# Kernel optimization log

Measured on AMD Instinct MI355X. Metric: run time of the kernel, lower is better.

## Reference

```python
import jax, jax.numpy as jnp
import numpy as np
from jax import lax

B, T, IN, H, DIM = 128, 1024, 64, 128, 64


def setup_inputs() -> dict:
    key = jax.random.key(0)
    ks = jax.random.split(key, 14)
    s = 0.05
    return {
        "x": jax.random.normal(ks[0], (B, T, IN), jnp.float32),
        "is_init": jax.random.randint(ks[1], (B, T, 1), 0, 2).astype(bool),
        "hx": jax.random.normal(ks[2], (B, H), jnp.float32),
        # MLP: Linear(IN,128) + ELU, Linear(128,128) + ELU
        "W1": jax.random.normal(ks[3], (128, IN), jnp.float32) * s,
        "b1": jnp.zeros((128,), jnp.float32),
        "W2": jax.random.normal(ks[4], (128, 128), jnp.float32) * s,
        "b2": jnp.zeros((128,), jnp.float32),
        # GRU params (torch layout: [3H, in] with gate order r,z,n)
        "W_ih": jax.random.normal(ks[5], (3 * H, 128), jnp.float32) * s,
        "b_ih": jnp.zeros((3 * H,), jnp.float32),
        "W_hh": jax.random.normal(ks[6], (3 * H, H), jnp.float32) * s,
        "b_hh": jnp.zeros((3 * H,), jnp.float32),
        # output head Linear(128, DIM)
        "W_out": jax.random.normal(ks[7], (DIM, 128), jnp.float32) * s,
        "b_out": jnp.zeros((DIM,), jnp.float32),
    }


def _gru_with_reset(xg, init_mask, h0, W_hh, b_hh):
    # xg: [T,B,3H] precomputed input-side gates; init_mask: [T,B,1] float
    def step(h, inp):
        xg_t, m_t = inp
        h = h * (1.0 - m_t)                       # reset hidden where is_init
        hg = h @ W_hh.T + b_hh                    # [B,3H]
        xr, xz, xn = jnp.split(xg_t, 3, axis=-1)
        hr, hz, hn = jnp.split(hg, 3, axis=-1)
        r = jax.nn.sigmoid(xr + hr)
        z = jax.nn.sigmoid(xz + hz)
        n = jnp.tanh(xn + r * hn)
        h_new = (1.0 - z) * n + z * h
        return h_new, h_new

    hT, ys = lax.scan(step, h0, (xg, init_mask))
    return ys, hT


def reference(x, is_init, hx, W1, b1, W2, b2, W_ih, b_ih, W_hh, b_hh, W_out, b_out):
    # MLP (ELU activations)
    h = jax.nn.elu(x @ W1.T + b1)
    h = jax.nn.elu(h @ W2.T + b2)                 # [B,T,128]
    # precompute input-side gate projections for all timesteps (one big GEMM)
    xg = h @ W_ih.T + b_ih                        # [B,T,3H]
    xg_t = jnp.transpose(xg, (1, 0, 2))           # [T,B,3H]
    m_t = jnp.transpose(is_init.astype(x.dtype), (1, 0, 2))  # [T,B,1]
    ys, hT = _gru_with_reset(xg_t, m_t, hx, W_hh, b_hh)
    y = jnp.transpose(ys, (1, 0, 2))              # [B,T,H]
    out = y @ W_out.T + b_out                     # [B,T,DIM]
    return out, hT
```

## Files before the change

### kernel.cpp

```cpp
#include <hip/hip_runtime.h>


#define T_SZ 1024

typedef __attribute__((ext_vector_type(8))) short short8;
typedef __attribute__((ext_vector_type(4))) float f32x4;
typedef unsigned long long u64;
typedef unsigned int uint32;

__device__ __forceinline__ unsigned short f2b(float f){
  return __builtin_bit_cast(unsigned short, (__bf16)f);
}
__device__ __forceinline__ float b2f(unsigned int hs){
  unsigned int u = hs << 16;
  return __builtin_bit_cast(float, u);
}
__device__ __forceinline__ short8 load_w8(const float* __restrict__ p){
  const float4* q = (const float4*)p;
  float4 u0 = q[0], u1 = q[1];
  short8 v;
  v[0]=(short)f2b(u0.x); v[1]=(short)f2b(u0.y); v[2]=(short)f2b(u0.z); v[3]=(short)f2b(u0.w);
  v[4]=(short)f2b(u1.x); v[5]=(short)f2b(u1.y); v[6]=(short)f2b(u1.z); v[7]=(short)f2b(u1.w);
  return v;
}
__device__ __forceinline__ float rcp_f(float x){ return __builtin_amdgcn_rcpf(x); }
__device__ __forceinline__ float elu(float v){ return v > 0.f ? v : __expf(v) - 1.f; }
__device__ __forceinline__ float sigm(float x){ return rcp_f(1.f + __expf(-x)); }
__device__ __forceinline__ float tanh_fast(float x){
  x = fminf(fmaxf(x, -15.f), 15.f);
  float e = __expf(-2.f * x);
  return (1.f - e) * rcp_f(1.f + e);
}
#define MFMA16(a,b,c) __builtin_amdgcn_mfma_f32_16x16x32_bf16(a, b, c, 0, 0, 0)


__global__ __launch_bounds__(512) void wprep(const float* __restrict__ Whh, uint4* __restrict__ wbf){
  int rec = blockIdx.x*512 + threadIdx.x;
  if(rec >= 6144) return;
  int q  = rec & 3;
  int n_ = (rec >> 2) & 127;
  int ks = (rec >> 9) & 3;
  int gt = rec >> 11;
  const float* p = Whh + (size_t)(n_ + 128*gt)*128 + ks*32 + q*8;
  uint4 o;
  o.x = (uint32)f2b(p[0]) | ((uint32)f2b(p[1]) << 16);
  o.y = (uint32)f2b(p[2]) | ((uint32)f2b(p[3]) << 16);
  o.z = (uint32)f2b(p[4]) | ((uint32)f2b(p[5]) << 16);
  o.w = (uint32)f2b(p[6]) | ((uint32)f2b(p[7]) << 16);
  wbf[rec] = o;
}

__global__ __launch_bounds__(512) void seg_build(const int* __restrict__ ii, uint32* C){
  __shared__ uint32 lh[1024];
  __shared__ uint32 lbase[1024];
  __shared__ uint32 ssum[512];
  __shared__ uint32 sbase;
  uint32* segs = C + 4096;
  const int tid = threadIdx.x;
  const int wv = tid >> 6, lane = tid & 63;
  const int b = blockIdx.x*8 + wv;

  for(int i = tid; i < 1024; i += 512) lh[i] = 0u;
  __syncthreads();

  u64 bal[16], mb[16];
  #pragma unroll
  for(int c=0;c<16;c++){
    int t = c*64 + lane;
    int m = ii[b*T_SZ + t];
    mb[c]  = __ballot(m != 0);
    bal[c] = __ballot((m != 0) || (t == 0));
  }
  int fsA[16]; int nx = T_SZ;
  #pragma unroll
  for(int c=15;c>=0;c--){ fsA[c]=nx; if(bal[c]) nx = c*64 + __builtin_ctzll(bal[c]); }

  int lenA[16], tA[16], rkA[16];
  #pragma unroll
  for(int c=0;c<16;c++){
    lenA[c] = 0;
    if((bal[c] >> lane) & 1ull){
      int t = c*64 + lane;
      u64 hi = (lane < 63) ? (bal[c] >> (lane+1)) : 0ull;
      int nxt = hi ? (t + 1 + __builtin_ctzll(hi)) : fsA[c];
      int len = nxt - t;
      int rst = (int)((mb[c] >> lane) & 1ull);
      len -= rst; t += rst;
      if(len > 0){
        lenA[c] = len; tA[c] = t;
        rkA[c] = (int)atomicAdd(&lh[1024 - len], 1u);
      }
    }
  }
  __syncthreads();

  uint32 c0 = lh[2*tid], c1 = lh[2*tid+1];
  ssum[tid] = c0 + c1;
  __syncthreads();
  #pragma unroll
  for(int off=1; off<512; off<<=1){
    uint32 v = (tid >= off) ? ssum[tid-off] : 0u;
    __syncthreads();
    ssum[tid] += v;
    __syncthreads();
  }
  uint32 excl = tid ? ssum[tid-1] : 0u;
  lbase[2*tid]   = excl;
  lbase[2*tid+1] = excl + c0;
  uint32 total = ssum[511];
  uint32 padded = (total + 15u) & ~15u;
  if(tid == 0){
    sbase = atomicAdd(&C[2], padded);
    atomicAdd(&C[1], padded >> 4);
  }
  __syncthreads();
  const uint32 base = sbase;

  #pragma unroll
  for(int c=0;c<16;c++){
    if(lenA[c] > 0){
      uint32 slot = base + lbase[1024 - lenA[c]] + (uint32)rkA[c];
      segs[slot] = ((uint32)b << 21) | ((uint32)tA[c] << 11) | (uint32)lenA[c];
    }
  }
  for(uint32 i = total + tid; i < padded; i += 512) segs[base + i] = 0u;
}

__global__ __launch_bounds__(512) void fused_mlp(
    const float* __restrict__ x, const int* __restrict__ ii,
    const float* __restrict__ W1, const float* __restrict__ b1,
    const float* __restrict__ W2, const float* __restrict__ b2,
    const float* __restrict__ Wih, const float* __restrict__ bih,
    const float* __restrict__ bhh,
    unsigned short* __restrict__ xg, unsigned short* __restrict__ ys,
    float* __restrict__ hT)
{
  __shared__ __align__(16) char smem[71680];
  unsigned short* xs0 = (unsigned short*)smem;
  unsigned short* xs1 = (unsigned short*)(smem + 18432);
  unsigned short* h1l = (unsigned short*)(smem + 36864);
  unsigned short* h2l = (unsigned short*)(smem + 54272);
  __shared__ int iil[2][64];
  const int tid = threadIdx.x;
  const int wv = tid >> 6, l = tid & 63, quad = l >> 4, col = l & 15;
  const int n = 16*wv + col;

  short8 w1f[2], w2f[4], wif[3][4];
  #pragma unroll
  for(int ks=0; ks<2; ks++) w1f[ks] = load_w8(W1 + n*64  + ks*32 + quad*8);
  #pragma unroll
  for(int ks=0; ks<4; ks++) w2f[ks] = load_w8(W2 + n*128 + ks*32 + quad*8);
  #pragma unroll
  for(int gt=0; gt<3; gt++){
    #pragma unroll
    for(int ks=0; ks<4; ks++)
      wif[gt][ks] = load_w8(Wih + (n + 128*gt)*128 + ks*32 + quad*8);
  }
  const float b1v = b1[n], b2v = b2[n];
  float bihv[3], bhhv[3];
  #pragma unroll
  for(int gt=0; gt<3; gt++){ bihv[gt] = bih[n + 128*gt]; bhhv[gt] = bhh[n + 128*gt]; }

  const int srow = tid >> 5, sk = tid & 31;

  auto stage3 = [&](int g3, int t03, const int* __restrict__ iilp){
    uint32 xgo[4];
    #pragma unroll
    for(int r=0; r<4; r++)
      xgo[r] = (((uint32)(16*g3 + quad*4 + r) << 10) + (uint32)t03) * 384u + (uint32)n;
    #pragma unroll
    for(int tt=0; tt<4; tt++){
      f32x4 a0 = {bihv[0], bihv[0], bihv[0], bihv[0]};
      f32x4 a1 = {bihv[1], bihv[1], bihv[1], bihv[1]};
      f32x4 a2 = {bihv[2], bihv[2], bihv[2], bihv[2]};
      #pragma unroll
      for(int ks=0; ks<4; ks++){
        short8 a = *(const short8*)&h2l[(tt*16 + col)*136 + ks*32 + quad*8];
        a0 = MFMA16(a, wif[0][ks], a0);
        a1 = MFMA16(a, wif[1][ks], a1);
        a2 = MFMA16(a, wif[2][ks], a2);
      }
      const int t = t03 + tt;
      #pragma unroll
      for(int r=0; r<4; r++){
        int row = quad*4 + r;
        unsigned short* p = xg + xgo[r] + (uint32)(tt*384);
        p[0]   = f2b(a0[r]);
        p[128] = f2b(a1[r]);
        p[256] = f2b(a2[r]);
        if(iilp[tt*16 + row] != 0){
          float rr = sigm(a0[r] + bhhv[0]);
          float zz = sigm(a1[r] + bhhv[1]);
          float nn = tanh_fast(a2[r] + rr*bhhv[2]);
          float h1 = (1.f - zz)*nn;
          ys[((size_t)(t*8 + g3)*16 + row)*128 + n] = f2b(h1);
          if(t == T_SZ-1)
            hT[(16*g3 + row)*128 + n] = h1;
        }
      }
    }
  };

  int have_prev = 0, pg = 0, pt0 = 0, p = 0;
  for(int tile = blockIdx.x; tile < 2048; tile += gridDim.x){
    const int g = tile & 7, t0 = (tile >> 3) * 4;
    unsigned short* xs = p ? xs1 : xs0;
    const float* src = x + (size_t)(16*g + srow)*(T_SZ*64) + (size_t)t0*64;
    float4 v0 = ((const float4*)src)[sk];
    float4 v1 = ((const float4*)src)[sk + 32];
    int iv = 0;
    if(tid < 64) iv = ii[(16*g + (tid & 15))*T_SZ + t0 + (tid >> 4)];
    if(have_prev) stage3(pg, pt0, iil[p^1]);
    {
      int s0 = sk, tt0 = s0 >> 4, k0 = (s0 & 15)*4;
      unsigned short* d0 = xs + (tt0*16 + srow)*72 + k0;
      d0[0]=f2b(v0.x); d0[1]=f2b(v0.y); d0[2]=f2b(v0.z); d0[3]=f2b(v0.w);
      int s1 = sk + 32, tt1 = s1 >> 4, k1 = (s1 & 15)*4;
      unsigned short* d1 = xs + (tt1*16 + srow)*72 + k1;
      d1[0]=f2b(v1.x); d1[1]=f2b(v1.y); d1[2]=f2b(v1.z); d1[3]=f2b(v1.w);
    }
    if(tid < 64) iil[p][tid] = iv;
    __syncthreads();
    #pragma unroll
    for(int tt=0; tt<4; tt++){
      f32x4 acc = {b1v, b1v, b1v, b1v};
      #pragma unroll
      for(int ks=0; ks<2; ks++){
        short8 a = *(const short8*)&xs[(tt*16 + col)*72 + ks*32 + quad*8];
        acc = MFMA16(a, w1f[ks], acc);
      }
      #pragma unroll
      for(int r=0; r<4; r++)
        h1l[(tt*16 + quad*4 + r)*136 + n] = f2b(elu(acc[r]));
    }
    __syncthreads();
    #pragma unroll
    for(int tt=0; tt<4; tt++){
      f32x4 acc = {b2v, b2v, b2v, b2v};
      #pragma unroll
      for(int ks=0; ks<4; ks++){
        short8 a = *(const short8*)&h1l[(tt*16 + col)*136 + ks*32 + quad*8];
        acc = MFMA16(a, w2f[ks], acc);
      }
      #pragma unroll
      for(int r=0; r<4; r++)
        h2l[(tt*16 + quad*4 + r)*136 + n] = f2b(elu(acc[r]));
    }
    __syncthreads();
    have_prev = 1; pg = g; pt0 = t0; p ^= 1;
  }
  if(have_prev) stage3(pg, pt0, iil[p^1]);
}

__global__ __launch_bounds__(512) void gru_seg_scan(
    const unsigned short* __restrict__ xg,
    const float* __restrict__ hx,
    const uint4* __restrict__ wbf, const float* __restrict__ bhh,
    const uint32* __restrict__ C,
    unsigned short* __restrict__ ys, float* __restrict__ hT)
{
  __shared__ unsigned short hl[2][16*136];
  __shared__ unsigned short xbuf[2][16*772];
  __shared__ int srb[16], srt[16], srlen[16];
  const uint32 ntile = C[1];
  const uint32 tile = blockIdx.x;
  if(tile >= ntile) return;

  const int tid = threadIdx.x;
  const int wv = tid >> 6, l = tid & 63, quad = l >> 4, col = l & 15;
  const int nidx = 16*wv + col;
  const int frow = tid >> 5, fk = tid & 31;
  const uint32* segs = C + 4096;

  short8 whf[3][4];
  float bhv[3];
  #pragma unroll
  for(int gt=0; gt<3; gt++){
    bhv[gt] = bhh[nidx + 128*gt];
    #pragma unroll
    for(int ks=0; ks<4; ks++){
      uint4 w = wbf[((gt*4 + ks)*128 + nidx)*4 + quad];
      whf[gt][ks] = __builtin_bit_cast(short8, w);
    }
  }

  if(tid < 16){
    uint32 w = segs[16*tile + (uint32)tid];
    srb[tid] = (int)(w >> 21);
    srt[tid] = (int)((w >> 11) & 1023u);
    srlen[tid] = (int)(w & 2047u);
  }
  __syncthreads();
  const int maxlen = srlen[0];
  const int fb = srb[frow], ft = srt[frow], fl = srlen[frow];

  float hreg[4];
  #pragma unroll
  for(int r=0; r<4; r++){
    int row = quad*4 + r;
    int b = srb[row], t0 = srt[row];
    float h0 = 0.f;
    if(srlen[row] > 0){
      h0 = (t0 == 0) ? hx[b*128 + nidx]
                     : b2f(ys[((size_t)((t0-1)*8 + (b>>4))*16 + (b&15))*128 + nidx]);
    }
    hreg[r] = h0;
    hl[0][row*136 + nidx] = f2b(h0);
  }
  {
    const unsigned short* src = xg + ((size_t)fb*T_SZ + ft)*384;
    unsigned short* xb = &xbuf[0][frow*772];
    #pragma unroll
    for(int i2=0; i2<3; i2++)
      *(u64*)(xb + i2*128 + fk*4) = *(const u64*)(src + i2*128 + fk*4);
  }

  int cur = 0;
  for(int i=0; i<maxlen; i++){
    __syncthreads();
    short8 af[4];
    #pragma unroll
    for(int ks=0; ks<4; ks++)
      af[ks] = *(const short8*)&hl[cur][col*136 + ks*32 + quad*8];
    f32x4 ar = {bhv[0], bhv[0], bhv[0], bhv[0]};
    f32x4 az = {bhv[1], bhv[1], bhv[1], bhv[1]};
    f32x4 an = {bhv[2], bhv[2], bhv[2], bhv[2]};
    #pragma unroll
    for(int ks=0; ks<4; ks++){
      ar = MFMA16(af[ks], whf[0][ks], ar);
      az = MFMA16(af[ks], whf[1][ks], az);
      an = MFMA16(af[ks], whf[2][ks], an);
    }
    u64 p0, p1, p2;
    {
      int tc = (i+1 < fl) ? i+1 : (fl > 0 ? fl-1 : 0);
      const unsigned short* src = xg + ((size_t)fb*T_SZ + (ft + tc))*384;
      p0 = *(const u64*)(src +       fk*4);
      p1 = *(const u64*)(src + 128 + fk*4);
      p2 = *(const u64*)(src + 256 + fk*4);
    }
    if(i >= 1 && i <= fl){
      int t = ft + i - 1;
      u64 hv = *(const u64*)&hl[cur][frow*136 + fk*4];
      *(u64*)(ys + ((size_t)(t*8 + (fb>>4))*16 + (fb&15))*128 + fk*4) = hv;
      if(i == fl && ft + fl == T_SZ){
        #pragma unroll
        for(int j=0; j<4; j++)
          hT[fb*128 + fk*4 + j] = b2f(hl[cur][frow*136 + fk*4 + j]);
      }
    }
    const unsigned short* xb = &xbuf[cur][0];
    #pragma unroll
    for(int r=0; r<4; r++){
      int row = quad*4 + r;
      float xrv = b2f(xb[row*772 +       nidx]);
      float xzv = b2f(xb[row*772 + 128 + nidx]);
      float xnv = b2f(xb[row*772 + 256 + nidx]);
      float rr = sigm(xrv + ar[r]);
      float zz = sigm(xzv + az[r]);
      float nn = tanh_fast(xnv + rr*an[r]);
      float hnew = (1.f - zz)*nn + zz*hreg[r];
      hreg[r] = hnew;
      hl[cur^1][row*136 + nidx] = f2b(hnew);
    }
    {
      unsigned short* xb2 = &xbuf[cur^1][frow*772];
      *(u64*)(xb2 +       fk*4) = p0;
      *(u64*)(xb2 + 128 + fk*4) = p1;
      *(u64*)(xb2 + 256 + fk*4) = p2;
    }
    cur ^= 1;
  }
  __syncthreads();
  if(maxlen >= 1 && fl == maxlen){
    int t = ft + maxlen - 1;
    u64 hv = *(const u64*)&hl[cur][frow*136 + fk*4];
    *(u64*)(ys + ((size_t)(t*8 + (fb>>4))*16 + (fb&15))*128 + fk*4) = hv;
    if(ft + fl == T_SZ){
      #pragma unroll
      for(int j=0; j<4; j++)
        hT[fb*128 + fk*4 + j] = b2f(hl[cur][frow*136 + fk*4 + j]);
    }
  }
}

__global__ __launch_bounds__(256) void out_gemm(
    const unsigned short* __restrict__ ys,
    const float* __restrict__ Wout, const float* __restrict__ bout,
    float* __restrict__ outp)
{
  const int tid = threadIdx.x;
  const int wv = tid >> 6, l = tid & 63, quad = l >> 4, col = l & 15;
  const int n = 16*wv + col;
  short8 wof[4];
  #pragma unroll
  for(int ks=0; ks<4; ks++) wof[ks] = load_w8(Wout + n*128 + ks*32 + quad*8);
  const float bov = bout[n];
  for(int tile = blockIdx.x; tile < 8192; tile += gridDim.x){
    const int t = tile >> 3, g = tile & 7;
    const unsigned short* yt = ys + (size_t)tile * 16 * 128;
    f32x4 acc = {bov, bov, bov, bov};
    #pragma unroll
    for(int ks=0; ks<4; ks++){
      short8 a = *(const short8*)&yt[col*128 + ks*32 + quad*8];
      acc = MFMA16(a, wof[ks], acc);
    }
    #pragma unroll
    for(int r=0; r<4; r++)
      outp[(size_t)(16*g + quad*4 + r)*(T_SZ*64) + (size_t)t*64 + n] = acc[r];
  }
}

extern "C" void kernel_launch(void* const* d_in, const int* in_sizes, int n_in,
                              void* d_out, int out_size, void* d_ws, size_t ws_size,
                              hipStream_t stream)
{
  const float* x    = (const float*)d_in[0];
  const int*   ii   = (const int*)  d_in[1];
  const float* hx   = (const float*)d_in[2];
  const float* W1   = (const float*)d_in[3];
  const float* b1   = (const float*)d_in[4];
  const float* W2   = (const float*)d_in[5];
  const float* b2   = (const float*)d_in[6];
  const float* Wih  = (const float*)d_in[7];
  const float* bih  = (const float*)d_in[8];
  const float* Whh  = (const float*)d_in[9];
  const float* bhh  = (const float*)d_in[10];
  const float* Wout = (const float*)d_in[11];
  const float* bout = (const float*)d_in[12];

  float* outp = (float*)d_out;
  float* hT   = outp + (size_t)128 * T_SZ * 64;
  uint32* C   = (uint32*)d_out;
  uint4* wbf  = (uint4*)((char*)d_out + (1u<<20));

  unsigned short* xg = (unsigned short*)d_ws;
  unsigned short* ys = (unsigned short*)((char*)d_ws + 100663296ull);

  hipMemsetAsync(C, 0, 64, stream);
  wprep      <<<dim3(12),   dim3(512),  0, stream>>>(Whh, wbf);
  seg_build  <<<dim3(16),   dim3(512),  0, stream>>>(ii, C);
  fused_mlp  <<<dim3(512),  dim3(512),  0, stream>>>(x, ii, W1, b1, W2, b2, Wih, bih, bhh, xg, ys, hT);
  gru_seg_scan<<<dim3(4160),dim3(512),  0, stream>>>(xg, hx, wbf, bhh, C, ys, hT);
  out_gemm   <<<dim3(2048), dim3(256),  0, stream>>>(ys, Wout, bout, outp);
}
```

Before: 235.0 us.

## Merge prep kernels, prebake bf16 weights, skip xg stores, shrink LDS, tune scan barrier

New measurement: 221.0 us. 1.06x faster.

```diff
diff --git a/kernel.cpp b/kernel.cpp
--- a/kernel.cpp
+++ b/kernel.cpp
@@ -14,14 +14,6 @@
 __device__ __forceinline__ float b2f(unsigned int hs){
   unsigned int u = hs << 16;
   return __builtin_bit_cast(float, u);
-}
-__device__ __forceinline__ short8 load_w8(const float* __restrict__ p){
-  const float4* q = (const float4*)p;
-  float4 u0 = q[0], u1 = q[1];
-  short8 v;
-  v[0]=(short)f2b(u0.x); v[1]=(short)f2b(u0.y); v[2]=(short)f2b(u0.z); v[3]=(short)f2b(u0.w);
-  v[4]=(short)f2b(u1.x); v[5]=(short)f2b(u1.y); v[6]=(short)f2b(u1.z); v[7]=(short)f2b(u1.w);
-  return v;
 }
 __device__ __forceinline__ float rcp_f(float x){ return __builtin_amdgcn_rcpf(x); }
 __device__ __forceinline__ float elu(float v){ return v > 0.f ? v : __expf(v) - 1.f; }
@@ -34,104 +26,128 @@
 #define MFMA16(a,b,c) __builtin_amdgcn_mfma_f32_16x16x32_bf16(a, b, c, 0, 0, 0)
 
 
-__global__ __launch_bounds__(512) void wprep(const float* __restrict__ Whh, uint4* __restrict__ wbf){
-  int rec = blockIdx.x*512 + threadIdx.x;
-  if(rec >= 6144) return;
-  int q  = rec & 3;
-  int n_ = (rec >> 2) & 127;
-  int ks = (rec >> 9) & 3;
-  int gt = rec >> 11;
-  const float* p = Whh + (size_t)(n_ + 128*gt)*128 + ks*32 + q*8;
-  uint4 o;
-  o.x = (uint32)f2b(p[0]) | ((uint32)f2b(p[1]) << 16);
-  o.y = (uint32)f2b(p[2]) | ((uint32)f2b(p[3]) << 16);
-  o.z = (uint32)f2b(p[4]) | ((uint32)f2b(p[5]) << 16);
-  o.w = (uint32)f2b(p[6]) | ((uint32)f2b(p[7]) << 16);
-  wbf[rec] = o;
-}
-
-__global__ __launch_bounds__(512) void seg_build(const int* __restrict__ ii, uint32* C){
-  __shared__ uint32 lh[1024];
-  __shared__ uint32 lbase[1024];
-  __shared__ uint32 ssum[512];
-  __shared__ uint32 sbase;
-  uint32* segs = C + 4096;
-  const int tid = threadIdx.x;
-  const int wv = tid >> 6, lane = tid & 63;
-  const int b = blockIdx.x*8 + wv;
-
-  for(int i = tid; i < 1024; i += 512) lh[i] = 0u;
-  __syncthreads();
-
-  u64 bal[16], mb[16];
-  #pragma unroll
-  for(int c=0;c<16;c++){
-    int t = c*64 + lane;
-    int m = ii[b*T_SZ + t];
-    mb[c]  = __ballot(m != 0);
-    bal[c] = __ballot((m != 0) || (t == 0));
-  }
-  int fsA[16]; int nx = T_SZ;
-  #pragma unroll
-  for(int c=15;c>=0;c--){ fsA[c]=nx; if(bal[c]) nx = c*64 + __builtin_ctzll(bal[c]); }
-
-  int lenA[16], tA[16], rkA[16];
-  #pragma unroll
-  for(int c=0;c<16;c++){
-    lenA[c] = 0;
-    if((bal[c] >> lane) & 1ull){
+__global__ __launch_bounds__(512) void prep(
+    const float* __restrict__ Whh, const float* __restrict__ W1,
+    const float* __restrict__ W2,  const float* __restrict__ Wih,
+    uint4* __restrict__ wtab, const int* __restrict__ ii, uint32* C)
+{
+  if(blockIdx.x < 30){
+    int rec = blockIdx.x*512 + threadIdx.x;
+    if(rec >= 15360) return;
+    const float* p;
+    if(rec < 6144){
+      int q = rec & 3, n_ = (rec >> 2) & 127, ks = (rec >> 9) & 3, gt = rec >> 11;
+      p = Whh + (size_t)(n_ + 128*gt)*128 + ks*32 + q*8;
+    } else if(rec < 7168){
+      int r = rec - 6144;
+      int q = r & 3, n_ = (r >> 2) & 127, ks = r >> 9;
+      p = W1 + (size_t)n_*64 + ks*32 + q*8;
+    } else if(rec < 9216){
+      int r = rec - 7168;
+      int q = r & 3, n_ = (r >> 2) & 127, ks = r >> 9;
+      p = W2 + (size_t)n_*128 + ks*32 + q*8;
+    } else {
+      int r = rec - 9216;
+      int q = r & 3, n_ = (r >> 2) & 127, ks = (r >> 9) & 3, gt = r >> 11;
+      p = Wih + (size_t)(n_ + 128*gt)*128 + ks*32 + q*8;
+    }
+    uint4 o;
+    o.x = (uint32)f2b(p[0]) | ((uint32)f2b(p[1]) << 16);
+    o.y = (uint32)f2b(p[2]) | ((uint32)f2b(p[3]) << 16);
+    o.z = (uint32)f2b(p[4]) | ((uint32)f2b(p[5]) << 16);
+    o.w = (uint32)f2b(p[6]) | ((uint32)f2b(p[7]) << 16);
+    wtab[rec] = o;
+  } else {
+    __shared__ uint32 lh[1024];
+    __shared__ uint32 lbase[1024];
+    __shared__ uint32 wsum[8];
+    __shared__ uint32 woff[8];
+    __shared__ uint32 stot;
+    __shared__ uint32 sbase;
+    uint32* segs = C + 4096;
+    const int tid = threadIdx.x;
+    const int wv = tid >> 6, lane = tid & 63;
+    const int b = (blockIdx.x - 30)*8 + wv;
+
+    for(int i = tid; i < 1024; i += 512) lh[i] = 0u;
+    __syncthreads();
+
+    u64 bal[16], mb[16];
+    #pragma unroll
+    for(int c=0;c<16;c++){
       int t = c*64 + lane;
-      u64 hi = (lane < 63) ? (bal[c] >> (lane+1)) : 0ull;
-      int nxt = hi ? (t + 1 + __builtin_ctzll(hi)) : fsA[c];
-      int len = nxt - t;
-      int rst = (int)((mb[c] >> lane) & 1ull);
-      len -= rst; t += rst;
-      if(len > 0){
-        lenA[c] = len; tA[c] = t;
-        rkA[c] = (int)atomicAdd(&lh[1024 - len], 1u);
-      }
-    }
-  }
-  __syncthreads();
-
-  uint32 c0 = lh[2*tid], c1 = lh[2*tid+1];
-  ssum[tid] = c0 + c1;
-  __syncthreads();
-  #pragma unroll
-  for(int off=1; off<512; off<<=1){
-    uint32 v = (tid >= off) ? ssum[tid-off] : 0u;
-    __syncthreads();
-    ssum[tid] += v;
-    __syncthreads();
-  }
-  uint32 excl = tid ? ssum[tid-1] : 0u;
-  lbase[2*tid]   = excl;
-  lbase[2*tid+1] = excl + c0;
-  uint32 total = ssum[511];
-  uint32 padded = (total + 15u) & ~15u;
-  if(tid == 0){
-    sbase = atomicAdd(&C[2], padded);
-    atomicAdd(&C[1], padded >> 4);
-  }
-  __syncthreads();
-  const uint32 base = sbase;
-
-  #pragma unroll
-  for(int c=0;c<16;c++){
-    if(lenA[c] > 0){
-      uint32 slot = base + lbase[1024 - lenA[c]] + (uint32)rkA[c];
-      segs[slot] = ((uint32)b << 21) | ((uint32)tA[c] << 11) | (uint32)lenA[c];
-    }
-  }
-  for(uint32 i = total + tid; i < padded; i += 512) segs[base + i] = 0u;
+      int m = ii[b*T_SZ + t];
+      mb[c]  = __ballot(m != 0);
+      bal[c] = __ballot((m != 0) || (t == 0));
+    }
+    int fsA[16]; int nx = T_SZ;
+    #pragma unroll
+    for(int c=15;c>=0;c--){ fsA[c]=nx; if(bal[c]) nx = c*64 + __builtin_ctzll(bal[c]); }
+
+    int lenA[16], tA[16], rkA[16];
+    #pragma unroll
+    for(int c=0;c<16;c++){
+      lenA[c] = 0;
+      if((bal[c] >> lane) & 1ull){
+        int t = c*64 + lane;
+        u64 hi = (lane < 63) ? (bal[c] >> (lane+1)) : 0ull;
+        int nxt = hi ? (t + 1 + __builtin_ctzll(hi)) : fsA[c];
+        int len = nxt - t;
+        int rst = (int)((mb[c] >> lane) & 1ull);
+        len -= rst; t += rst;
+        if(len > 0){
+          lenA[c] = len; tA[c] = t;
+          rkA[c] = (int)atomicAdd(&lh[1024 - len], 1u);
+        }
+      }
+    }
+    __syncthreads();
+
+    uint32 c0 = lh[2*tid], c1 = lh[2*tid+1];
+    uint32 v = c0 + c1;
+    uint32 incl = v;
+    #pragma unroll
+    for(int d=1; d<64; d<<=1){
+      uint32 t = __shfl_up(incl, d);
+      if(lane >= d) incl += t;
+    }
+    if(lane == 63) wsum[wv] = incl;
+    __syncthreads();
+    if(tid < 8){
+      uint32 s = 0;
+      for(int k=0; k<tid; k++) s += wsum[k];
+      woff[tid] = s;
+      if(tid == 7) stot = s + wsum[7];
+    }
+    __syncthreads();
+    uint32 excl = incl + woff[wv] - v;
+    lbase[2*tid]   = excl;
+    lbase[2*tid+1] = excl + c0;
+    uint32 total = stot;
+    uint32 padded = (total + 15u) & ~15u;
+    if(tid == 0){
+      sbase = atomicAdd(&C[2], padded);
+      atomicAdd(&C[1], padded >> 4);
+    }
+    __syncthreads();
+    const uint32 base = sbase;
+
+    #pragma unroll
+    for(int c=0;c<16;c++){
+      if(lenA[c] > 0){
+        uint32 slot = base + lbase[1024 - lenA[c]] + (uint32)rkA[c];
+        segs[slot] = ((uint32)b << 21) | ((uint32)tA[c] << 11) | (uint32)lenA[c];
+      }
+    }
+    for(uint32 i = total + tid; i < padded; i += 512) segs[base + i] = 0u;
+  }
 }
 
 __global__ __launch_bounds__(512) void fused_mlp(
     const float* __restrict__ x, const int* __restrict__ ii,
-    const float* __restrict__ W1, const float* __restrict__ b1,
-    const float* __restrict__ W2, const float* __restrict__ b2,
-    const float* __restrict__ Wih, const float* __restrict__ bih,
-    const float* __restrict__ bhh,
+    const uint4* __restrict__ wtab,
+    const float* __restrict__ b1, const float* __restrict__ b2,
+    const float* __restrict__ bih, const float* __restrict__ bhh,
     unsigned short* __restrict__ xg, unsigned short* __restrict__ ys,
     float* __restrict__ hT)
 {
@@ -147,14 +163,16 @@
 
   short8 w1f[2], w2f[4], wif[3][4];
   #pragma unroll
-  for(int ks=0; ks<2; ks++) w1f[ks] = load_w8(W1 + n*64  + ks*32 + quad*8);
-  #pragma unroll
-  for(int ks=0; ks<4; ks++) w2f[ks] = load_w8(W2 + n*128 + ks*32 + quad*8);
+  for(int ks=0; ks<2; ks++)
+    w1f[ks] = __builtin_bit_cast(short8, wtab[6144 + (ks*128 + n)*4 + quad]);
+  #pragma unroll
+  for(int ks=0; ks<4; ks++)
+    w2f[ks] = __builtin_bit_cast(short8, wtab[7168 + (ks*128 + n)*4 + quad]);
   #pragma unroll
   for(int gt=0; gt<3; gt++){
     #pragma unroll
     for(int ks=0; ks<4; ks++)
-      wif[gt][ks] = load_w8(Wih + (n + 128*gt)*128 + ks*32 + quad*8);
+      wif[gt][ks] = __builtin_bit_cast(short8, wtab[9216 + ((gt*4 + ks)*128 + n)*4 + quad]);
   }
   const float b1v = b1[n], b2v = b2[n];
   float bihv[3], bhhv[3];
@@ -184,10 +202,6 @@
       #pragma unroll
       for(int r=0; r<4; r++){
         int row = quad*4 + r;
-        unsigned short* p = xg + xgo[r] + (uint32)(tt*384);
-        p[0]   = f2b(a0[r]);
-        p[128] = f2b(a1[r]);
-        p[256] = f2b(a2[r]);
         if(iilp[tt*16 + row] != 0){
           float rr = sigm(a0[r] + bhhv[0]);
           float zz = sigm(a1[r] + bhhv[1]);
@@ -196,6 +210,11 @@
           ys[((size_t)(t*8 + g3)*16 + row)*128 + n] = f2b(h1);
           if(t == T_SZ-1)
             hT[(16*g3 + row)*128 + n] = h1;
+        } else {
+          unsigned short* p = xg + xgo[r] + (uint32)(tt*384);
+          p[0]   = f2b(a0[r]);
+          p[128] = f2b(a1[r]);
+          p[256] = f2b(a2[r]);
         }
       }
     }
@@ -214,10 +233,12 @@
     {
       int s0 = sk, tt0 = s0 >> 4, k0 = (s0 & 15)*4;
       unsigned short* d0 = xs + (tt0*16 + srow)*72 + k0;
-      d0[0]=f2b(v0.x); d0[1]=f2b(v0.y); d0[2]=f2b(v0.z); d0[3]=f2b(v0.w);
+      u64 w0 = (u64)f2b(v0.x) | ((u64)f2b(v0.y)<<16) | ((u64)f2b(v0.z)<<32) | ((u64)f2b(v0.w)<<48);
+      *(u64*)d0 = w0;
       int s1 = sk + 32, tt1 = s1 >> 4, k1 = (s1 & 15)*4;
       unsigned short* d1 = xs + (tt1*16 + srow)*72 + k1;
-      d1[0]=f2b(v1.x); d1[1]=f2b(v1.y); d1[2]=f2b(v1.z); d1[3]=f2b(v1.w);
+      u64 w1 = (u64)f2b(v1.x) | ((u64)f2b(v1.y)<<16) | ((u64)f2b(v1.z)<<32) | ((u64)f2b(v1.w)<<48);
+      *(u64*)d1 = w1;
     }
     if(tid < 64) iil[p][tid] = iv;
     __syncthreads();
@@ -260,7 +281,7 @@
     unsigned short* __restrict__ ys, float* __restrict__ hT)
 {
   __shared__ unsigned short hl[2][16*136];
-  __shared__ unsigned short xbuf[2][16*772];
+  __shared__ unsigned short xbuf[2][16*388];
   __shared__ int srb[16], srt[16], srlen[16];
   const uint32 ntile = C[1];
   const uint32 tile = blockIdx.x;
@@ -309,7 +330,7 @@
   }
   {
     const unsigned short* src = xg + ((size_t)fb*T_SZ + ft)*384;
-    unsigned short* xb = &xbuf[0][frow*772];
+    unsigned short* xb = &xbuf[0][frow*388];
     #pragma unroll
     for(int i2=0; i2<3; i2++)
       *(u64*)(xb + i2*128 + fk*4) = *(const u64*)(src + i2*128 + fk*4);
@@ -317,7 +338,10 @@
 
   int cur = 0;
   for(int i=0; i<maxlen; i++){
-    __syncthreads();
+    asm volatile("s_waitcnt lgkmcnt(0)" ::: "memory");
+    __builtin_amdgcn_s_barrier();
+    __builtin_amdgcn_sched_barrier(0);
+    __builtin_amdgcn_s_setprio(1);
     short8 af[4];
     #pragma unroll
     for(int ks=0; ks<4; ks++)
@@ -331,6 +355,7 @@
       az = MFMA16(af[ks], whf[1][ks], az);
       an = MFMA16(af[ks], whf[2][ks], an);
     }
+    __builtin_amdgcn_s_setprio(0);
     u64 p0, p1, p2;
     {
       int tc = (i+1 < fl) ? i+1 : (fl > 0 ? fl-1 : 0);
@@ -353,9 +378,9 @@
     #pragma unroll
     for(int r=0; r<4; r++){
       int row = quad*4 + r;
-      float xrv = b2f(xb[row*772 +       nidx]);
-      float xzv = b2f(xb[row*772 + 128 + nidx]);
-      float xnv = b2f(xb[row*772 + 256 + nidx]);
+      float xrv = b2f(xb[row*388 +       nidx]);
+      float xzv = b2f(xb[row*388 + 128 + nidx]);
+      float xnv = b2f(xb[row*388 + 256 + nidx]);
       float rr = sigm(xrv + ar[r]);
       float zz = sigm(xzv + az[r]);
       float nn = tanh_fast(xnv + rr*an[r]);
@@ -364,7 +389,7 @@
       hl[cur^1][row*136 + nidx] = f2b(hnew);
     }
     {
-      unsigned short* xb2 = &xbuf[cur^1][frow*772];
+      unsigned short* xb2 = &xbuf[cur^1][frow*388];
       *(u64*)(xb2 +       fk*4) = p0;
       *(u64*)(xb2 + 128 + fk*4) = p1;
       *(u64*)(xb2 + 256 + fk*4) = p2;
@@ -394,7 +419,15 @@
   const int n = 16*wv + col;
   short8 wof[4];
   #pragma unroll
-  for(int ks=0; ks<4; ks++) wof[ks] = load_w8(Wout + n*128 + ks*32 + quad*8);
+  for(int ks=0; ks<4; ks++){
+    const float* p = Wout + n*128 + ks*32 + quad*8;
+    const float4* q = (const float4*)p;
+    float4 u0 = q[0], u1 = q[1];
+    short8 v;
+    v[0]=(short)f2b(u0.x); v[1]=(short)f2b(u0.y); v[2]=(short)f2b(u0.z); v[3]=(short)f2b(u0.w);
+    v[4]=(short)f2b(u1.x); v[5]=(short)f2b(u1.y); v[6]=(short)f2b(u1.z); v[7]=(short)f2b(u1.w);
+    wof[ks] = v;
+  }
   const float bov = bout[n];
   for(int tile = blockIdx.x; tile < 8192; tile += gridDim.x){
     const int t = tile >> 3, g = tile & 7;
@@ -432,15 +465,14 @@
   float* outp = (float*)d_out;
   float* hT   = outp + (size_t)128 * T_SZ * 64;
   uint32* C   = (uint32*)d_out;
-  uint4* wbf  = (uint4*)((char*)d_out + (1u<<20));
+  uint4* wtab = (uint4*)((char*)d_out + (1u<<20));
 
   unsigned short* xg = (unsigned short*)d_ws;
   unsigned short* ys = (unsigned short*)((char*)d_ws + 100663296ull);
 
   hipMemsetAsync(C, 0, 64, stream);
-  wprep      <<<dim3(12),   dim3(512),  0, stream>>>(Whh, wbf);
-  seg_build  <<<dim3(16),   dim3(512),  0, stream>>>(ii, C);
-  fused_mlp  <<<dim3(512),  dim3(512),  0, stream>>>(x, ii, W1, b1, W2, b2, Wih, bih, bhh, xg, ys, hT);
-  gru_seg_scan<<<dim3(4160),dim3(512),  0, stream>>>(xg, hx, wbf, bhh, C, ys, hT);
+  prep       <<<dim3(46),   dim3(512),  0, stream>>>(Whh, W1, W2, Wih, wtab, ii, C);
+  fused_mlp  <<<dim3(512),  dim3(512),  0, stream>>>(x, ii, wtab, b1, b2, bih, bhh, xg, ys, hT);
+  gru_seg_scan<<<dim3(4160),dim3(512),  0, stream>>>(xg, hx, wtab, bhh, C, ys, hT);
   out_gemm   <<<dim3(2048), dim3(256),  0, stream>>>(ys, Wout, bout, outp);
 }
```
